# Optimization experiments

Hardware: AMD Instinct MI355X
Metric: run time of the kernel (lower is better)

The kernel has to match this reference:

```python
import jax, jax.numpy as jnp
import numpy as np

C_IN = 256
C_KEY = 128
C_VAL = 256


def setup_inputs() -> dict:
    key = jax.random.key(0)
    ks = jax.random.split(key, 10)
    B, H, W = 8, 64, 64
    s_in = 1.0 / np.sqrt(C_IN)
    s_val = 1.0 / np.sqrt(C_VAL)
    return {
        "x": jax.random.normal(ks[0], (B, C_IN, H, W), jnp.float32),
        "Wk": jax.random.uniform(ks[1], (C_KEY, C_IN), jnp.float32, -s_in, s_in),
        "bk": jax.random.uniform(ks[2], (C_KEY,), jnp.float32, -s_in, s_in),
        "Wq": jax.random.uniform(ks[3], (C_KEY, C_IN), jnp.float32, -s_in, s_in),
        "bq": jax.random.uniform(ks[4], (C_KEY,), jnp.float32, -s_in, s_in),
        "Wv": jax.random.uniform(ks[5], (C_VAL, C_IN), jnp.float32, -s_in, s_in),
        "bv": jax.random.uniform(ks[6], (C_VAL,), jnp.float32, -s_in, s_in),
        "Wr": jax.random.uniform(ks[7], (C_IN, C_VAL), jnp.float32, -s_val, s_val),
        "br": jax.random.uniform(ks[8], (C_IN,), jnp.float32, -s_val, s_val),
        "gamma": jnp.zeros((1,), jnp.float32) + 0.5,  # nonzero so attention path is exercised
    }


def reference(x, Wk, bk, Wq, bq, Wv, bv, Wr, br, gamma):
    B, C, H, W = x.shape
    N = H * W
    xf = x.reshape(B, C, N)  # [B, C, N]
    # 1x1 convs == per-pixel linear projections
    k = jnp.einsum('kc,bcn->bkn', Wk, xf) + bk[None, :, None]   # [B, Ck, N]
    q = jnp.einsum('kc,bcn->bkn', Wq, xf) + bq[None, :, None]   # [B, Ck, N]
    v = jnp.einsum('vc,bcn->bvn', Wv, xf) + bv[None, :, None]   # [B, Cv, N]
    # attention = q^T k, softmax over keys (no scaling, per original)
    att = jnp.einsum('bkq,bkn->bqn', q, k)                      # [B, N, N]
    att = jax.nn.softmax(att, axis=-1)
    out = jnp.einsum('bvn,bqn->bvq', v, att)                    # [B, Cv, N]
    out = jnp.einsum('cv,bvn->bcn', Wr, out) + br[None, :, None]
    out = out.reshape(B, C, H, W)
    return gamma * out + x
```

## Files before the change

### kernel.cpp

```cpp
#include <hip/hip_runtime.h>
#include <hip/hip_bf16.h>
#include <stdint.h>

#define NPIX 4096

typedef __attribute__((ext_vector_type(8))) short bf16x8;
typedef __attribute__((ext_vector_type(16))) float f32x16;
typedef __attribute__((ext_vector_type(4))) unsigned int uint4v;

__device__ __forceinline__ unsigned short bfb(float f) {
  __hip_bfloat16 h = __float2bfloat16(f);
  return __builtin_bit_cast(unsigned short, h);
}
__device__ __forceinline__ unsigned pack2(float a, float b) {
  return (unsigned)bfb(a) | ((unsigned)bfb(b) << 16);
}
__device__ __forceinline__ f32x16 mfma32(bf16x8 a, bf16x8 b, f32x16 c) {
  return __builtin_amdgcn_mfma_f32_32x32x16_bf16(a, b, c, 0, 0, 0);
}

__global__ void k_cvt(const float* __restrict__ Wq, const float* __restrict__ Wk,
                      const float* __restrict__ Wv, const float* __restrict__ Wr,
                      unsigned short* __restrict__ wqk, unsigned short* __restrict__ wv,
                      unsigned short* __restrict__ wr) {
  int i = blockIdx.x * 256 + threadIdx.x;
  wqk[i] = bfb(i < 32768 ? Wq[i] : Wk[i - 32768]);
  wv[i]  = bfb(Wv[i]);
  wr[i]  = bfb(Wr[i]);
}

__launch_bounds__(256, 2)
__global__ void k_qkv(const float* __restrict__ x,
                      const unsigned short* __restrict__ wqk,
                      const unsigned short* __restrict__ wv,
                      const float* __restrict__ bq, const float* __restrict__ bk,
                      const float* __restrict__ bv,
                      unsigned short* __restrict__ qT, unsigned short* __restrict__ kT,
                      unsigned short* __restrict__ vV) {
  __shared__ __align__(16) unsigned short xT[64 * 256];
  const int b = blockIdx.x & 7;
  const int n0 = (blockIdx.x >> 3) * 64;
  const int t = threadIdx.x;
  const float* xb = x + (size_t)b * 256 * NPIX;
  #pragma unroll
  for (int p = 0; p < 16; ++p) {
    int c = (t >> 4) + p * 16;
    int nq = (t & 15) * 4;
    float4 f = *reinterpret_cast<const float4*>(xb + (size_t)c * NPIX + n0 + nq);
    float vals[4] = {f.x, f.y, f.z, f.w};
    #pragma unroll
    for (int j = 0; j < 4; ++j) {
      int n = nq + j;
      int byteoff = n * 512 + ((c * 2) ^ ((n & 7) << 4));
      xT[byteoff >> 1] = bfb(vals[j]);
    }
  }
  __syncthreads();
  const int lane = t & 63, w = t >> 6, l31 = lane & 31, hi = lane >> 5;
  f32x16 aq[2][2], av[2][2];
  #pragma unroll
  for (int a0 = 0; a0 < 2; ++a0)
    #pragma unroll
    for (int a1 = 0; a1 < 2; ++a1)
      #pragma unroll
      for (int i = 0; i < 16; ++i) { aq[a0][a1][i] = 0.f; av[a0][a1][i] = 0.f; }
  #pragma unroll
  for (int s = 0; s < 16; ++s) {
    bf16x8 xa[2];
    #pragma unroll
    for (int nt = 0; nt < 2; ++nt) {
      int n = nt * 32 + l31;
      int byteoff = n * 512 + (((s * 32 + hi * 16)) ^ ((n & 7) << 4));
      xa[nt] = *reinterpret_cast<const bf16x8*>(reinterpret_cast<const char*>(xT) + byteoff);
    }
    #pragma unroll
    for (int oc2 = 0; oc2 < 2; ++oc2) {
      int oc = w * 64 + oc2 * 32 + l31;
      bf16x8 wq = *reinterpret_cast<const bf16x8*>(wqk + oc * 256 + s * 16 + hi * 8);
      bf16x8 wvf = *reinterpret_cast<const bf16x8*>(wv + oc * 256 + s * 16 + hi * 8);
      #pragma unroll
      for (int nt = 0; nt < 2; ++nt) {
        aq[oc2][nt] = mfma32(xa[nt], wq, aq[oc2][nt]);
        av[oc2][nt] = mfma32(wvf, xa[nt], av[oc2][nt]);
      }
    }
  }
  #pragma unroll
  for (int oc2 = 0; oc2 < 2; ++oc2) {
    int oc = w * 64 + oc2 * 32 + l31;
    float bias = (oc < 128) ? bq[oc] : bk[oc - 128];
    unsigned short* dst = (oc < 128) ? (qT + (size_t)b * NPIX * 128 + oc)
                                     : (kT + (size_t)b * NPIX * 128 + (oc - 128));
    #pragma unroll
    for (int nt = 0; nt < 2; ++nt)
      #pragma unroll
      for (int r = 0; r < 16; ++r) {
        int n = n0 + nt * 32 + (r & 3) + 8 * (r >> 2) + 4 * hi;
        dst[(size_t)n * 128] = bfb(aq[oc2][nt][r] + bias);
      }
  }
  unsigned short* vb = vV + (size_t)b * 256 * NPIX;
  #pragma unroll
  for (int vc2 = 0; vc2 < 2; ++vc2)
    #pragma unroll
    for (int nt = 0; nt < 2; ++nt)
      #pragma unroll
      for (int r = 0; r < 16; ++r) {
        int vc = w * 64 + vc2 * 32 + (r & 3) + 8 * (r >> 2) + 4 * hi;
        int n = n0 + nt * 32 + l31;
        vb[(size_t)vc * NPIX + n] = bfb(av[vc2][nt][r] + bv[vc]);
      }
}

__launch_bounds__(256, 1)
__global__ void k_attn(const unsigned short* __restrict__ qT,
                       const unsigned short* __restrict__ kT,
                       const unsigned short* __restrict__ vV,
                       unsigned short* __restrict__ oT) {
  __shared__ __align__(16) unsigned short Kl[64 * 128];
  __shared__ __align__(16) unsigned short Vl[256 * 64];
  const int b = blockIdx.x & 7;
  const int qt = blockIdx.x >> 3;
  const int t = threadIdx.x, w = t >> 6, lane = t & 63, l31 = lane & 31, hi = lane >> 5;
  const int qp = qt * 128 + w * 32 + l31;
  const unsigned short* qTb = qT + (size_t)b * NPIX * 128;
  const unsigned short* kTb = kT + (size_t)b * NPIX * 128;
  const unsigned short* vb  = vV + (size_t)b * 256 * NPIX;
  bf16x8 qf[8];
  #pragma unroll
  for (int s = 0; s < 8; ++s)
    qf[s] = *reinterpret_cast<const bf16x8*>(qTb + (size_t)qp * 128 + s * 16 + hi * 8);
  f32x16 O[8];
  #pragma unroll
  for (int vt = 0; vt < 8; ++vt)
    #pragma unroll
    for (int i = 0; i < 16; ++i) O[vt][i] = 0.f;
  float m_run = -3.0e38f, l_run = 0.0f;

  for (int kt = 0; kt < 64; ++kt) {
    const int kp0 = kt * 64;
    #pragma unroll
    for (int i = 0; i < 4; ++i) {
      int row = w * 16 + i * 4 + (lane >> 4);
      int c2 = (lane & 15) * 16;
      uint4v d = *reinterpret_cast<const uint4v*>(
          reinterpret_cast<const char*>(kTb) + (size_t)(kp0 + row) * 256 + c2);
      *reinterpret_cast<uint4v*>(reinterpret_cast<char*>(Kl) + row * 256 + (c2 ^ ((row & 7) << 4))) = d;
    }
    #pragma unroll
    for (int i = 0; i < 8; ++i) {
      int vc = w * 64 + i * 8 + (lane >> 3);
      int c2 = (lane & 7) * 16;
      uint4v d = *reinterpret_cast<const uint4v*>(
          reinterpret_cast<const char*>(vb) + (size_t)vc * 8192 + kp0 * 2 + c2);
      *reinterpret_cast<uint4v*>(reinterpret_cast<char*>(Vl) + vc * 128 + (c2 ^ ((vc & 7) << 4))) = d;
    }
    __syncthreads();
    #pragma unroll
    for (int rt = 0; rt < 2; ++rt) {
      f32x16 S;
      #pragma unroll
      for (int i = 0; i < 16; ++i) S[i] = 0.f;
      #pragma unroll
      for (int s = 0; s < 8; ++s) {
        int row = rt * 32 + l31;
        int byteoff = row * 256 + ((s * 32 + hi * 16) ^ ((row & 7) << 4));
        bf16x8 ka = *reinterpret_cast<const bf16x8*>(reinterpret_cast<const char*>(Kl) + byteoff);
        S = mfma32(ka, qf[s], S);
      }
      float mx = S[0];
      #pragma unroll
      for (int i = 1; i < 16; ++i) mx = fmaxf(mx, S[i]);
      mx = fmaxf(mx, __shfl_xor(mx, 32));
      if (__any(mx > m_run + 8.0f)) {
        float mn = fmaxf(m_run, mx);
        float al = __expf(m_run - mn);
        l_run *= al;
        #pragma unroll
        for (int vt = 0; vt < 8; ++vt)
          #pragma unroll
          for (int i = 0; i < 16; ++i) O[vt][i] *= al;
        m_run = mn;
      }
      float p[16], sum = 0.f;
      #pragma unroll
      for (int i = 0; i < 16; ++i) { p[i] = __expf(S[i] - m_run); sum += p[i]; }
      sum += __shfl_xor(sum, 32);
      l_run += sum;
      unsigned wd[8];
      #pragma unroll
      for (int i = 0; i < 8; ++i) wd[i] = pack2(p[2 * i], p[2 * i + 1]);
      #pragma unroll
      for (int pr = 0; pr < 4; ++pr) {
        int ia = (pr & 1) + (pr >> 1) * 4;
        int ib = ia + 2;
        unsigned xs = (unsigned)__shfl_xor((int)wd[ia], 32);
        unsigned ys = (unsigned)__shfl_xor((int)wd[ib], 32);
        unsigned na = hi ? ys : wd[ia];
        unsigned nb = hi ? wd[ib] : xs;
        wd[ia] = na; wd[ib] = nb;
      }
      bf16x8 pf[2];
      { uint4v u; u.x = wd[0]; u.y = wd[1]; u.z = wd[2]; u.w = wd[3];
        pf[0] = __builtin_bit_cast(bf16x8, u); }
      { uint4v u; u.x = wd[4]; u.y = wd[5]; u.z = wd[6]; u.w = wd[7];
        pf[1] = __builtin_bit_cast(bf16x8, u); }
      #pragma unroll
      for (int sl = 0; sl < 2; ++sl) {
        #pragma unroll
        for (int vt = 0; vt < 8; ++vt) {
          int vc = vt * 32 + l31;
          int byteoff = vc * 128 + (((rt * 2 + sl) * 32 + hi * 16) ^ ((vc & 7) << 4));
          bf16x8 va = *reinterpret_cast<const bf16x8*>(reinterpret_cast<const char*>(Vl) + byteoff);
          O[vt] = mfma32(va, pf[sl], O[vt]);
        }
      }
    }
    __syncthreads();
  }
  float rl = 1.0f / l_run;
  unsigned short* oTb = oT + (size_t)b * NPIX * 256;
  #pragma unroll
  for (int vt = 0; vt < 8; ++vt)
    #pragma unroll
    for (int i = 0; i < 16; i += 2) {
      int vc = vt * 32 + (i & 3) + 8 * (i >> 2) + 4 * hi;
      unsigned pk = pack2(O[vt][i] * rl, O[vt][i + 1] * rl);
      *reinterpret_cast<unsigned*>(oTb + (size_t)qp * 256 + vc) = pk;
    }
}

__launch_bounds__(256, 2)
__global__ void k_out(const unsigned short* __restrict__ oT,
                      const unsigned short* __restrict__ wr,
                      const float* __restrict__ br, const float* __restrict__ gamma,
                      const float* __restrict__ x, float* __restrict__ out) {
  const int b = blockIdx.x & 7;
  const int n0 = (blockIdx.x >> 3) * 64;
  const int t = threadIdx.x, w = t >> 6, lane = t & 63, l31 = lane & 31, hi = lane >> 5;
  const unsigned short* oTb = oT + (size_t)b * NPIX * 256;
  f32x16 acc[2][2];
  #pragma unroll
  for (int a0 = 0; a0 < 2; ++a0)
    #pragma unroll
    for (int a1 = 0; a1 < 2; ++a1)
      #pragma unroll
      for (int i = 0; i < 16; ++i) acc[a0][a1][i] = 0.f;
  #pragma unroll
  for (int s = 0; s < 16; ++s) {
    bf16x8 ofr[2], wfr[2];
    #pragma unroll
    for (int nt = 0; nt < 2; ++nt) {
      int n = n0 + nt * 32 + l31;
      ofr[nt] = *reinterpret_cast<const bf16x8*>(oTb + (size_t)n * 256 + s * 16 + hi * 8);
    }
    #pragma unroll
    for (int c2 = 0; c2 < 2; ++c2) {
      int c = w * 64 + c2 * 32 + l31;
      wfr[c2] = *reinterpret_cast<const bf16x8*>(wr + c * 256 + s * 16 + hi * 8);
    }
    #pragma unroll
    for (int c2 = 0; c2 < 2; ++c2)
      #pragma unroll
      for (int nt = 0; nt < 2; ++nt)
        acc[c2][nt] = mfma32(wfr[c2], ofr[nt], acc[c2][nt]);
  }
  float g = gamma[0];
  #pragma unroll
  for (int c2 = 0; c2 < 2; ++c2)
    #pragma unroll
    for (int nt = 0; nt < 2; ++nt)
      #pragma unroll
      for (int r = 0; r < 16; ++r) {
        int c = w * 64 + c2 * 32 + (r & 3) + 8 * (r >> 2) + 4 * hi;
        int n = n0 + nt * 32 + l31;
        size_t idx = (size_t)b * 256 * NPIX + (size_t)c * NPIX + n;
        out[idx] = g * (acc[c2][nt][r] + br[c]) + x[idx];
      }
}

extern "C" void kernel_launch(void* const* d_in, const int* in_sizes, int n_in,
                              void* d_out, int out_size, void* d_ws, size_t ws_size,
                              hipStream_t stream) {
  const float* x     = (const float*)d_in[0];
  const float* Wk    = (const float*)d_in[1];
  const float* bk    = (const float*)d_in[2];
  const float* Wq    = (const float*)d_in[3];
  const float* bq    = (const float*)d_in[4];
  const float* Wv    = (const float*)d_in[5];
  const float* bv    = (const float*)d_in[6];
  const float* Wr    = (const float*)d_in[7];
  const float* br    = (const float*)d_in[8];
  const float* gamma = (const float*)d_in[9];

  const size_t OFF_QT  = 0;
  const size_t OFF_KT  = 8388608;
  const size_t OFF_V   = 16777216;
  const size_t OFF_OT  = 33554432;
  const size_t OFF_WQK = 50331648;
  const size_t OFF_WV  = 50462720;
  const size_t OFF_WR  = 50593792;
  const size_t NEED    = 50724864;
  if (ws_size < NEED) return;

  char* ws = (char*)d_ws;
  unsigned short* qT  = (unsigned short*)(ws + OFF_QT);
  unsigned short* kT  = (unsigned short*)(ws + OFF_KT);
  unsigned short* vV  = (unsigned short*)(ws + OFF_V);
  unsigned short* oT  = (unsigned short*)(ws + OFF_OT);
  unsigned short* wqk = (unsigned short*)(ws + OFF_WQK);
  unsigned short* wvb = (unsigned short*)(ws + OFF_WV);
  unsigned short* wrb = (unsigned short*)(ws + OFF_WR);

  k_cvt<<<256, 256, 0, stream>>>(Wq, Wk, Wv, Wr, wqk, wvb, wrb);
  k_qkv<<<512, 256, 0, stream>>>(x, wqk, wvb, bq, bk, bv, qT, kT, vV);
  k_attn<<<256, 256, 0, stream>>>(qT, kT, vV, oT);
  k_out<<<512, 256, 0, stream>>>(oT, wrb, br, gamma, x, (float*)d_out);
}
```

Measured before the change: 224.5 us.

## Split attention key range across two wave groups per block and merge partial softmax

Doubles the attention block to 512 threads. Two groups of four waves each process half of the key sequence for the same 128 queries, each group with its own K/V shared-memory tiles. The partial O, max and sum from the second group are merged into the first through shared memory in two rounds, doing the flash-decoding style rescale. The intent is more waves per CU to hide latency with the same 256-block grid. It also adds s_setprio around the MFMA sections and a tree max reduction, at the cost of a merge epilogue, larger shared memory and higher register pressure under the new launch bounds.

Measured after the change: 268.5 us. 19.6% more time.

```diff
diff --git a/kernel.cpp b/kernel.cpp
--- a/kernel.cpp
+++ b/kernel.cpp
@@ -112,17 +112,19 @@
       }
 }
 
-__launch_bounds__(256, 1)
+__launch_bounds__(512, 2)
 __global__ void k_attn(const unsigned short* __restrict__ qT,
                        const unsigned short* __restrict__ kT,
                        const unsigned short* __restrict__ vV,
                        unsigned short* __restrict__ oT) {
-  __shared__ __align__(16) unsigned short Kl[64 * 128];
-  __shared__ __align__(16) unsigned short Vl[256 * 64];
+  __shared__ __align__(16) char smem[98304];
   const int b = blockIdx.x & 7;
   const int qt = blockIdx.x >> 3;
-  const int t = threadIdx.x, w = t >> 6, lane = t & 63, l31 = lane & 31, hi = lane >> 5;
-  const int qp = qt * 128 + w * 32 + l31;
+  const int t = threadIdx.x, lane = t & 63, l31 = lane & 31, hi = lane >> 5;
+  const int w = t >> 6, h = w >> 2, sw = w & 3;
+  char* Kl = smem + h * 49152;
+  char* Vl = smem + h * 49152 + 16384;
+  const int qp = qt * 128 + sw * 32 + l31;
   const unsigned short* qTb = qT + (size_t)b * NPIX * 128;
   const unsigned short* kTb = kT + (size_t)b * NPIX * 128;
   const unsigned short* vb  = vV + (size_t)b * 256 * NPIX;
@@ -137,23 +139,23 @@
     for (int i = 0; i < 16; ++i) O[vt][i] = 0.f;
   float m_run = -3.0e38f, l_run = 0.0f;
 
-  for (int kt = 0; kt < 64; ++kt) {
-    const int kp0 = kt * 64;
+  for (int kt2 = 0; kt2 < 32; ++kt2) {
+    const int kp0 = (h * 32 + kt2) * 64;
     #pragma unroll
     for (int i = 0; i < 4; ++i) {
-      int row = w * 16 + i * 4 + (lane >> 4);
+      int row = sw * 16 + i * 4 + (lane >> 4);
       int c2 = (lane & 15) * 16;
       uint4v d = *reinterpret_cast<const uint4v*>(
           reinterpret_cast<const char*>(kTb) + (size_t)(kp0 + row) * 256 + c2);
-      *reinterpret_cast<uint4v*>(reinterpret_cast<char*>(Kl) + row * 256 + (c2 ^ ((row & 7) << 4))) = d;
+      *reinterpret_cast<uint4v*>(Kl + row * 256 + (c2 ^ ((row & 7) << 4))) = d;
     }
     #pragma unroll
     for (int i = 0; i < 8; ++i) {
-      int vc = w * 64 + i * 8 + (lane >> 3);
+      int vc = sw * 64 + i * 8 + (lane >> 3);
       int c2 = (lane & 7) * 16;
       uint4v d = *reinterpret_cast<const uint4v*>(
           reinterpret_cast<const char*>(vb) + (size_t)vc * 8192 + kp0 * 2 + c2);
-      *reinterpret_cast<uint4v*>(reinterpret_cast<char*>(Vl) + vc * 128 + (c2 ^ ((vc & 7) << 4))) = d;
+      *reinterpret_cast<uint4v*>(Vl + vc * 128 + (c2 ^ ((vc & 7) << 4))) = d;
     }
     __syncthreads();
     #pragma unroll
@@ -161,16 +163,19 @@
       f32x16 S;
       #pragma unroll
       for (int i = 0; i < 16; ++i) S[i] = 0.f;
+      __builtin_amdgcn_s_setprio(1);
       #pragma unroll
       for (int s = 0; s < 8; ++s) {
         int row = rt * 32 + l31;
         int byteoff = row * 256 + ((s * 32 + hi * 16) ^ ((row & 7) << 4));
-        bf16x8 ka = *reinterpret_cast<const bf16x8*>(reinterpret_cast<const char*>(Kl) + byteoff);
+        bf16x8 ka = *reinterpret_cast<const bf16x8*>(Kl + byteoff);
         S = mfma32(ka, qf[s], S);
       }
-      float mx = S[0];
-      #pragma unroll
-      for (int i = 1; i < 16; ++i) mx = fmaxf(mx, S[i]);
+      __builtin_amdgcn_s_setprio(0);
+      float mx = fmaxf(fmaxf(fmaxf(S[0], S[1]), fmaxf(S[2], S[3])),
+                       fmaxf(fmaxf(S[4], S[5]), fmaxf(S[6], S[7])));
+      mx = fmaxf(mx, fmaxf(fmaxf(fmaxf(S[8], S[9]), fmaxf(S[10], S[11])),
+                           fmaxf(fmaxf(S[12], S[13]), fmaxf(S[14], S[15]))));
       mx = fmaxf(mx, __shfl_xor(mx, 32));
       if (__any(mx > m_run + 8.0f)) {
         float mn = fmaxf(m_run, mx);
@@ -205,29 +210,73 @@
         pf[0] = __builtin_bit_cast(bf16x8, u); }
       { uint4v u; u.x = wd[4]; u.y = wd[5]; u.z = wd[6]; u.w = wd[7];
         pf[1] = __builtin_bit_cast(bf16x8, u); }
+      __builtin_amdgcn_s_setprio(1);
       #pragma unroll
       for (int sl = 0; sl < 2; ++sl) {
         #pragma unroll
         for (int vt = 0; vt < 8; ++vt) {
           int vc = vt * 32 + l31;
           int byteoff = vc * 128 + (((rt * 2 + sl) * 32 + hi * 16) ^ ((vc & 7) << 4));
-          bf16x8 va = *reinterpret_cast<const bf16x8*>(reinterpret_cast<const char*>(Vl) + byteoff);
+          bf16x8 va = *reinterpret_cast<const bf16x8*>(Vl + byteoff);
           O[vt] = mfma32(va, pf[sl], O[vt]);
         }
       }
+      __builtin_amdgcn_s_setprio(0);
     }
     __syncthreads();
   }
-  float rl = 1.0f / l_run;
-  unsigned short* oTb = oT + (size_t)b * NPIX * 256;
-  #pragma unroll
-  for (int vt = 0; vt < 8; ++vt)
-    #pragma unroll
-    for (int i = 0; i < 16; i += 2) {
-      int vc = vt * 32 + (i & 3) + 8 * (i >> 2) + 4 * hi;
-      unsigned pk = pack2(O[vt][i] * rl, O[vt][i + 1] * rl);
-      *reinterpret_cast<unsigned*>(oTb + (size_t)qp * 256 + vc) = pk;
-    }
+  float4* shf = (float4*)smem;
+  float* ml = (float*)(smem + 65536);
+  float a0 = 1.f, a1 = 0.f, rl = 1.f;
+  #pragma unroll 2
+  for (int round = 0; round < 2; ++round) {
+    if (h == 1) {
+      #pragma unroll
+      for (int vt4 = 0; vt4 < 4; ++vt4)
+        #pragma unroll
+        for (int i4 = 0; i4 < 4; ++i4) {
+          float4 f;
+          f.x = O[round * 4 + vt4][i4 * 4];
+          f.y = O[round * 4 + vt4][i4 * 4 + 1];
+          f.z = O[round * 4 + vt4][i4 * 4 + 2];
+          f.w = O[round * 4 + vt4][i4 * 4 + 3];
+          shf[((vt4 * 4 + i4) * 4 + sw) * 64 + lane] = f;
+        }
+      if (round == 0) { ml[sw * 64 + lane] = m_run; ml[256 + sw * 64 + lane] = l_run; }
+    }
+    __syncthreads();
+    if (h == 0) {
+      if (round == 0) {
+        float m1 = ml[sw * 64 + lane], l1 = ml[256 + sw * 64 + lane];
+        float m = fmaxf(m_run, m1);
+        a0 = __expf(m_run - m);
+        a1 = __expf(m1 - m);
+        rl = 1.0f / (l_run * a0 + l1 * a1);
+      }
+      #pragma unroll
+      for (int vt4 = 0; vt4 < 4; ++vt4)
+        #pragma unroll
+        for (int i4 = 0; i4 < 4; ++i4) {
+          float4 f = shf[((vt4 * 4 + i4) * 4 + sw) * 64 + lane];
+          O[round * 4 + vt4][i4 * 4]     = O[round * 4 + vt4][i4 * 4] * a0     + f.x * a1;
+          O[round * 4 + vt4][i4 * 4 + 1] = O[round * 4 + vt4][i4 * 4 + 1] * a0 + f.y * a1;
+          O[round * 4 + vt4][i4 * 4 + 2] = O[round * 4 + vt4][i4 * 4 + 2] * a0 + f.z * a1;
+          O[round * 4 + vt4][i4 * 4 + 3] = O[round * 4 + vt4][i4 * 4 + 3] * a0 + f.w * a1;
+        }
+    }
+    __syncthreads();
+  }
+  if (h == 0) {
+    unsigned short* oTb = oT + (size_t)b * NPIX * 256;
+    #pragma unroll
+    for (int vt = 0; vt < 8; ++vt)
+      #pragma unroll
+      for (int i = 0; i < 16; i += 2) {
+        int vc = vt * 32 + (i & 3) + 8 * (i >> 2) + 4 * hi;
+        unsigned pk = pack2(O[vt][i] * rl, O[vt][i + 1] * rl);
+        *reinterpret_cast<unsigned*>(oTb + (size_t)qp * 256 + vc) = pk;
+      }
+  }
 }
 
 __launch_bounds__(256, 2)
@@ -314,6 +363,6 @@
 
   k_cvt<<<256, 256, 0, stream>>>(Wq, Wk, Wv, Wr, wqk, wvb, wrb);
   k_qkv<<<512, 256, 0, stream>>>(x, wqk, wvb, bq, bk, bv, qT, kT, vV);
-  k_attn<<<256, 256, 0, stream>>>(qT, kT, vV, oT);
+  k_attn<<<256, 512, 0, stream>>>(qT, kT, vV, oT);
   k_out<<<512, 256, 0, stream>>>(oT, wrb, br, gamma, x, (float*)d_out);
 }
```

## Split attention block across value-channel halves and raise occupancy

Applied to the files above, without the earlier changes.

The attention kernel now covers 64 queries per block instead of 128. The four waves split two query halves by two value-channel halves, so each wave keeps four output accumulator tiles instead of eight. This doubles the grid to 512 blocks and allows up to three blocks per CU, aimed at better latency hiding and CU utilisation. It also adds s_setprio around the MFMA sections and a tree max reduction. The cost is that each QK^T score tile is now computed redundantly by two waves, and K/V tiles are loaded once per 64 queries rather than per 128.

Result: slower. 407.6 us (+81.6%).

```diff
diff --git a/kernel.cpp b/kernel.cpp
--- a/kernel.cpp
+++ b/kernel.cpp
@@ -112,17 +112,19 @@
       }
 }
 
-__launch_bounds__(256, 1)
+__launch_bounds__(256, 3)
 __global__ void k_attn(const unsigned short* __restrict__ qT,
                        const unsigned short* __restrict__ kT,
                        const unsigned short* __restrict__ vV,
                        unsigned short* __restrict__ oT) {
-  __shared__ __align__(16) unsigned short Kl[64 * 128];
-  __shared__ __align__(16) unsigned short Vl[256 * 64];
+  __shared__ __align__(16) char smem[49152];
   const int b = blockIdx.x & 7;
   const int qt = blockIdx.x >> 3;
-  const int t = threadIdx.x, w = t >> 6, lane = t & 63, l31 = lane & 31, hi = lane >> 5;
-  const int qp = qt * 128 + w * 32 + l31;
+  const int t = threadIdx.x, lane = t & 63, l31 = lane & 31, hi = lane >> 5;
+  const int sw = t >> 6, qh = sw & 1, vh = sw >> 1;
+  char* Kl = smem;
+  char* Vl = smem + 16384;
+  const int qp = qt * 64 + qh * 32 + l31;
   const unsigned short* qTb = qT + (size_t)b * NPIX * 128;
   const unsigned short* kTb = kT + (size_t)b * NPIX * 128;
   const unsigned short* vb  = vV + (size_t)b * 256 * NPIX;
@@ -130,9 +132,9 @@
   #pragma unroll
   for (int s = 0; s < 8; ++s)
     qf[s] = *reinterpret_cast<const bf16x8*>(qTb + (size_t)qp * 128 + s * 16 + hi * 8);
-  f32x16 O[8];
-  #pragma unroll
-  for (int vt = 0; vt < 8; ++vt)
+  f32x16 O[4];
+  #pragma unroll
+  for (int vt = 0; vt < 4; ++vt)
     #pragma unroll
     for (int i = 0; i < 16; ++i) O[vt][i] = 0.f;
   float m_run = -3.0e38f, l_run = 0.0f;
@@ -141,19 +143,19 @@
     const int kp0 = kt * 64;
     #pragma unroll
     for (int i = 0; i < 4; ++i) {
-      int row = w * 16 + i * 4 + (lane >> 4);
+      int row = sw * 16 + i * 4 + (lane >> 4);
       int c2 = (lane & 15) * 16;
       uint4v d = *reinterpret_cast<const uint4v*>(
           reinterpret_cast<const char*>(kTb) + (size_t)(kp0 + row) * 256 + c2);
-      *reinterpret_cast<uint4v*>(reinterpret_cast<char*>(Kl) + row * 256 + (c2 ^ ((row & 7) << 4))) = d;
+      *reinterpret_cast<uint4v*>(Kl + row * 256 + (c2 ^ ((row & 7) << 4))) = d;
     }
     #pragma unroll
     for (int i = 0; i < 8; ++i) {
-      int vc = w * 64 + i * 8 + (lane >> 3);
+      int vc = sw * 64 + i * 8 + (lane >> 3);
       int c2 = (lane & 7) * 16;
       uint4v d = *reinterpret_cast<const uint4v*>(
           reinterpret_cast<const char*>(vb) + (size_t)vc * 8192 + kp0 * 2 + c2);
-      *reinterpret_cast<uint4v*>(reinterpret_cast<char*>(Vl) + vc * 128 + (c2 ^ ((vc & 7) << 4))) = d;
+      *reinterpret_cast<uint4v*>(Vl + vc * 128 + (c2 ^ ((vc & 7) << 4))) = d;
     }
     __syncthreads();
     #pragma unroll
@@ -161,35 +163,38 @@
       f32x16 S;
       #pragma unroll
       for (int i = 0; i < 16; ++i) S[i] = 0.f;
+      __builtin_amdgcn_s_setprio(1);
       #pragma unroll
       for (int s = 0; s < 8; ++s) {
         int row = rt * 32 + l31;
         int byteoff = row * 256 + ((s * 32 + hi * 16) ^ ((row & 7) << 4));
-        bf16x8 ka = *reinterpret_cast<const bf16x8*>(reinterpret_cast<const char*>(Kl) + byteoff);
+        bf16x8 ka = *reinterpret_cast<const bf16x8*>(Kl + byteoff);
         S = mfma32(ka, qf[s], S);
       }
-      float mx = S[0];
-      #pragma unroll
-      for (int i = 1; i < 16; ++i) mx = fmaxf(mx, S[i]);
+      __builtin_amdgcn_s_setprio(0);
+      float mx = fmaxf(fmaxf(fmaxf(S[0], S[1]), fmaxf(S[2], S[3])),
+                       fmaxf(fmaxf(S[4], S[5]), fmaxf(S[6], S[7])));
+      mx = fmaxf(mx, fmaxf(fmaxf(fmaxf(S[8], S[9]), fmaxf(S[10], S[11])),
+                           fmaxf(fmaxf(S[12], S[13]), fmaxf(S[14], S[15]))));
       mx = fmaxf(mx, __shfl_xor(mx, 32));
       if (__any(mx > m_run + 8.0f)) {
         float mn = fmaxf(m_run, mx);
         float al = __expf(m_run - mn);
         l_run *= al;
         #pragma unroll
-        for (int vt = 0; vt < 8; ++vt)
+        for (int vt = 0; vt < 4; ++vt)
           #pragma unroll
           for (int i = 0; i < 16; ++i) O[vt][i] *= al;
         m_run = mn;
       }
-      float p[16], sum = 0.f;
-      #pragma unroll
-      for (int i = 0; i < 16; ++i) { p[i] = __expf(S[i] - m_run); sum += p[i]; }
+      float sum = 0.f;
+      #pragma unroll
+      for (int i = 0; i < 16; ++i) { S[i] = __expf(S[i] - m_run); sum += S[i]; }
       sum += __shfl_xor(sum, 32);
       l_run += sum;
       unsigned wd[8];
       #pragma unroll
-      for (int i = 0; i < 8; ++i) wd[i] = pack2(p[2 * i], p[2 * i + 1]);
+      for (int i = 0; i < 8; ++i) wd[i] = pack2(S[2 * i], S[2 * i + 1]);
       #pragma unroll
       for (int pr = 0; pr < 4; ++pr) {
         int ia = (pr & 1) + (pr >> 1) * 4;
@@ -205,26 +210,28 @@
         pf[0] = __builtin_bit_cast(bf16x8, u); }
       { uint4v u; u.x = wd[4]; u.y = wd[5]; u.z = wd[6]; u.w = wd[7];
         pf[1] = __builtin_bit_cast(bf16x8, u); }
+      __builtin_amdgcn_s_setprio(1);
       #pragma unroll
       for (int sl = 0; sl < 2; ++sl) {
         #pragma unroll
-        for (int vt = 0; vt < 8; ++vt) {
-          int vc = vt * 32 + l31;
+        for (int vt = 0; vt < 4; ++vt) {
+          int vc = vh * 128 + vt * 32 + l31;
           int byteoff = vc * 128 + (((rt * 2 + sl) * 32 + hi * 16) ^ ((vc & 7) << 4));
-          bf16x8 va = *reinterpret_cast<const bf16x8*>(reinterpret_cast<const char*>(Vl) + byteoff);
+          bf16x8 va = *reinterpret_cast<const bf16x8*>(Vl + byteoff);
           O[vt] = mfma32(va, pf[sl], O[vt]);
         }
       }
+      __builtin_amdgcn_s_setprio(0);
     }
     __syncthreads();
   }
   float rl = 1.0f / l_run;
   unsigned short* oTb = oT + (size_t)b * NPIX * 256;
   #pragma unroll
-  for (int vt = 0; vt < 8; ++vt)
+  for (int vt = 0; vt < 4; ++vt)
     #pragma unroll
     for (int i = 0; i < 16; i += 2) {
-      int vc = vt * 32 + (i & 3) + 8 * (i >> 2) + 4 * hi;
+      int vc = vh * 128 + vt * 32 + (i & 3) + 8 * (i >> 2) + 4 * hi;
       unsigned pk = pack2(O[vt][i] * rl, O[vt][i + 1] * rl);
       *reinterpret_cast<unsigned*>(oTb + (size_t)qp * 256 + vc) = pk;
     }
@@ -314,6 +321,6 @@
 
   k_cvt<<<256, 256, 0, stream>>>(Wq, Wk, Wv, Wr, wqk, wvb, wrb);
   k_qkv<<<512, 256, 0, stream>>>(x, wqk, wvb, bq, bk, bv, qT, kT, vV);
-  k_attn<<<256, 256, 0, stream>>>(qT, kT, vV, oT);
+  k_attn<<<512, 256, 0, stream>>>(qT, kT, vV, oT);
   k_out<<<512, 256, 0, stream>>>(oT, wrb, br, gamma, x, (float*)d_out);
 }
```
